# Kernel tuning notes

Measured on AMD Instinct MI355X. Metric: run time of the kernel, lower is better.

Reference implementation:

```python
import jax, jax.numpy as jnp
import numpy as np

B, S, HID = 2, 2048, 2048
NH = 16
HD = HID // NH  # 128


def setup_inputs() -> dict:
    key = jax.random.key(0)
    ks = jax.random.split(key, 9)
    w = 0.02  # init scale to keep logits in a sane range
    return {
        "hidden_states": jax.random.normal(ks[0], (B, S, HID), dtype=jnp.float32),
        "Wq": jax.random.normal(ks[1], (HID, HID), dtype=jnp.float32) * w,
        "bq": jnp.zeros((HID,), dtype=jnp.float32),
        "Wk": jax.random.normal(ks[2], (HID, HD), dtype=jnp.float32) * w,
        "bk": jnp.zeros((HD,), dtype=jnp.float32),
        "Wv": jax.random.normal(ks[3], (HID, HD), dtype=jnp.float32) * w,
        "bv": jnp.zeros((HD,), dtype=jnp.float32),
        "Wo": jax.random.normal(ks[4], (HID, HID), dtype=jnp.float32) * w,
        "bo": jnp.zeros((HID,), dtype=jnp.float32),
    }


def reference(hidden_states, Wq, bq, Wk, bk, Wv, bv, Wo, bo):
    b, s, _ = hidden_states.shape
    # Projections (weights stored [in, out])
    q = hidden_states @ Wq + bq                      # [B,S,HID]
    k = hidden_states @ Wk + bk                      # [B,S,HD] single shared KV head
    v = hidden_states @ Wv + bv                      # [B,S,HD]
    q = q.reshape(b, s, NH, HD)                      # [B,S,H,D]
    # MQA: all query heads attend to the same K/V
    scores = jnp.einsum("bshd,btd->bhst", q, k) / jnp.sqrt(jnp.float32(HD))  # [B,H,S,S]
    probs = jax.nn.softmax(scores, axis=-1)
    attn = jnp.einsum("bhst,btd->bshd", probs, v)    # [B,S,H,D]
    attn = attn.reshape(b, s, HID)
    return attn @ Wo + bo
```

## Files before the change

kernel.cpp:

```cpp
#include <hip/hip_runtime.h>
#include <math.h>

#define BB  2
#define SS  2048
#define HID 2048
#define NH  16
#define HD  128
#define MT  (BB * SS)
#define NC  (HID + 2 * HD)
#define QK_SCALE 0.08838834764831845f

typedef unsigned short ushort_t;
typedef unsigned int uint_t;
typedef __bf16 bf16x8 __attribute__((ext_vector_type(8)));
typedef short short8 __attribute__((ext_vector_type(8)));
typedef float f32x4 __attribute__((ext_vector_type(4)));

__device__ __forceinline__ ushort_t f2bf(float x) {
    union { float f; uint_t u; } a; a.f = x;
    return (ushort_t)((a.u + 0x7FFFu + ((a.u >> 16) & 1u)) >> 16);
}
__device__ __forceinline__ ushort_t f2bf_fast(float x) {
    union { float f; uint_t u; } a; a.f = x;
    return (ushort_t)((a.u + 0x8000u) >> 16);
}

__device__ __forceinline__ int sw_addr(int r, int c) {
    return ((r >> 1) << 6) + ((((((r & 1) << 2) | c)) ^ ((r >> 1) & 7)) << 3);
}

__global__ __launch_bounds__(256) void conv_bf16_kernel(
    const float* __restrict__ in, ushort_t* __restrict__ outb)
{
    const size_t i = ((size_t)blockIdx.x * 256 + threadIdx.x) * 8;
    const float4 a = *(const float4*)&in[i];
    const float4 b = *(const float4*)&in[i + 4];
    short8 o;
    o[0] = (short)f2bf(a.x); o[1] = (short)f2bf(a.y);
    o[2] = (short)f2bf(a.z); o[3] = (short)f2bf(a.w);
    o[4] = (short)f2bf(b.x); o[5] = (short)f2bf(b.y);
    o[6] = (short)f2bf(b.z); o[7] = (short)f2bf(b.w);
    *(short8*)&outb[i] = o;
}

__global__ __launch_bounds__(256) void convT_kernel(
    const float* __restrict__ W, ushort_t* __restrict__ Th, int K, int N)
{
    __shared__ float Ts[64][65];
    const int t = threadIdx.x;
    const int k0 = blockIdx.x * 64, n0 = blockIdx.y * 64;
    const int rr = t >> 4, c4 = (t & 15) * 4;
#pragma unroll
    for (int i = 0; i < 4; i++) {
        const int k = rr + i * 16;
        const float4 v = *(const float4*)&W[(size_t)(k0 + k) * N + n0 + c4];
        Ts[k][c4 + 0] = v.x; Ts[k][c4 + 1] = v.y;
        Ts[k][c4 + 2] = v.z; Ts[k][c4 + 3] = v.w;
    }
    __syncthreads();
    const int n = t >> 2, kc = (t & 3) * 16;
    short8 hv[2];
#pragma unroll
    for (int jj = 0; jj < 16; jj++)
        hv[jj >> 3][jj & 7] = (short)f2bf(Ts[kc + jj][n]);
    const size_t ob = (size_t)(n0 + n) * K + k0 + kc;
    *(short8*)&Th[ob]     = hv[0];
    *(short8*)&Th[ob + 8] = hv[1];
}

__global__ __launch_bounds__(256, 2) void gemm_qkv_kernel(
    const ushort_t* __restrict__ Ab, const ushort_t* __restrict__ WT,
    const float* __restrict__ bq, const float* __restrict__ bk,
    const float* __restrict__ bv,
    ushort_t* __restrict__ qb, ushort_t* __restrict__ kb,
    ushort_t* __restrict__ vtb)
{
    __shared__ short lds[8192];
    constexpr int AH = 0, BH = 4096;
    constexpr int K = HID;
    const int t  = threadIdx.x;
    const int wv = t >> 6, ln = t & 63;
    const int row0 = blockIdx.y * 128, col0 = blockIdx.x * 128;

    size_t agbase[2], bgbase[2];
    int    lbase[2];
#pragma unroll
    for (int i = 0; i < 2; i++) {
        const int I = wv * 2 + i;
        const int lrow = I * 8 + (ln >> 3);
        const int sb = (ln & 7) ^ (lrow & 7);
        const int rr = lrow * 2 + (sb >> 2);
        const int cc = sb & 3;
        agbase[i] = (size_t)(row0 + rr) * K + cc * 8;
        bgbase[i] = (size_t)(col0 + rr) * K + cc * 8;
        lbase[i] = I * 512;
    }

    const int wm0 = (wv & 1) * 64, wn0 = (wv >> 1) * 64;
    const int q = ln >> 4, lm = ln & 15;
    int aoff[4], boff[4];
#pragma unroll
    for (int i = 0; i < 4; i++) aoff[i] = sw_addr(wm0 + i * 16 + lm, q);
#pragma unroll
    for (int j = 0; j < 4; j++) boff[j] = sw_addr(wn0 + j * 16 + lm, q);

    f32x4 acc[4][4];
#pragma unroll
    for (int i = 0; i < 4; i++)
#pragma unroll
        for (int j = 0; j < 4; j++) acc[i][j] = 0.f;

    for (int k0 = 0; k0 < K; k0 += 32) {
        __syncthreads();
#pragma unroll
        for (int i = 0; i < 2; i++) {
            __builtin_amdgcn_global_load_lds(
                (const __attribute__((address_space(1))) void*)(Ab + agbase[i] + k0),
                (__attribute__((address_space(3))) void*)&lds[AH + lbase[i]], 16, 0, 0);
            __builtin_amdgcn_global_load_lds(
                (const __attribute__((address_space(1))) void*)(WT + bgbase[i] + k0),
                (__attribute__((address_space(3))) void*)&lds[BH + lbase[i]], 16, 0, 0);
        }
        __syncthreads();

        bf16x8 ah[4], bh[4];
#pragma unroll
        for (int i = 0; i < 4; i++) ah[i] = *(const bf16x8*)&lds[AH + aoff[i]];
#pragma unroll
        for (int j = 0; j < 4; j++) bh[j] = *(const bf16x8*)&lds[BH + boff[j]];
#pragma unroll
        for (int i = 0; i < 4; i++)
#pragma unroll
            for (int j = 0; j < 4; j++)
                acc[i][j] = __builtin_amdgcn_mfma_f32_16x16x32_bf16(ah[i], bh[j], acc[i][j], 0, 0, 0);
    }

    const int mode = (col0 < HID) ? 0 : ((col0 == HID) ? 1 : 2);
    const float* bsel = (mode == 0) ? bq : ((mode == 1) ? bk : bv);
    const int noff = (mode == 0) ? 0 : ((mode == 1) ? HID : HID + HD);
    float bj[4];
#pragma unroll
    for (int j = 0; j < 4; j++) bj[j] = bsel[col0 - noff + wn0 + j * 16 + lm];
#pragma unroll
    for (int i = 0; i < 4; i++) {
        const int mb = row0 + wm0 + i * 16 + q * 4;
#pragma unroll
        for (int j = 0; j < 4; j++) {
            const int nn = col0 + wn0 + j * 16 + lm;
#pragma unroll
            for (int rr2 = 0; rr2 < 4; rr2++) {
                const float v = acc[i][j][rr2] + bj[j];
                if (mode == 0)      qb [(size_t)(mb + rr2) * HID + nn]           = f2bf_fast(v * QK_SCALE);
                else if (mode == 1) kb [(size_t)(mb + rr2) * HD + (nn - HID)]    = f2bf_fast(v);
                else                vtb[(size_t)(nn - HID - HD) * MT + mb + rr2] = f2bf_fast(v);
            }
        }
    }
}

__global__ __launch_bounds__(256, 2) void gemm_oproj_kernel(
    const ushort_t* __restrict__ Ab, const ushort_t* __restrict__ WT,
    const float* __restrict__ bias, float* __restrict__ C, int M, int N, int K)
{
    __shared__ short lds[8192];
    constexpr int AH = 0, BH = 4096;
    const int t  = threadIdx.x;
    const int wv = t >> 6, ln = t & 63;
    const int row0 = blockIdx.y * 128, col0 = blockIdx.x * 128;

    size_t agbase[2], bgbase[2];
    int    lbase[2];
#pragma unroll
    for (int i = 0; i < 2; i++) {
        const int I = wv * 2 + i;
        const int lrow = I * 8 + (ln >> 3);
        const int sb = (ln & 7) ^ (lrow & 7);
        const int rr = lrow * 2 + (sb >> 2);
        const int cc = sb & 3;
        agbase[i] = (size_t)(row0 + rr) * K + cc * 8;
        bgbase[i] = (size_t)(col0 + rr) * K + cc * 8;
        lbase[i] = I * 512;
    }

    const int wm0 = (wv & 1) * 64, wn0 = (wv >> 1) * 64;
    const int q = ln >> 4, lm = ln & 15;
    int aoff[4], boff[4];
#pragma unroll
    for (int i = 0; i < 4; i++) aoff[i] = sw_addr(wm0 + i * 16 + lm, q);
#pragma unroll
    for (int j = 0; j < 4; j++) boff[j] = sw_addr(wn0 + j * 16 + lm, q);

    f32x4 acc[4][4];
#pragma unroll
    for (int i = 0; i < 4; i++)
#pragma unroll
        for (int j = 0; j < 4; j++) acc[i][j] = 0.f;

    for (int k0 = 0; k0 < K; k0 += 32) {
        __syncthreads();
#pragma unroll
        for (int i = 0; i < 2; i++) {
            __builtin_amdgcn_global_load_lds(
                (const __attribute__((address_space(1))) void*)(Ab + agbase[i] + k0),
                (__attribute__((address_space(3))) void*)&lds[AH + lbase[i]], 16, 0, 0);
            __builtin_amdgcn_global_load_lds(
                (const __attribute__((address_space(1))) void*)(WT + bgbase[i] + k0),
                (__attribute__((address_space(3))) void*)&lds[BH + lbase[i]], 16, 0, 0);
        }
        __syncthreads();

        bf16x8 ah[4], bh[4];
#pragma unroll
        for (int i = 0; i < 4; i++) ah[i] = *(const bf16x8*)&lds[AH + aoff[i]];
#pragma unroll
        for (int j = 0; j < 4; j++) bh[j] = *(const bf16x8*)&lds[BH + boff[j]];
#pragma unroll
        for (int i = 0; i < 4; i++)
#pragma unroll
            for (int j = 0; j < 4; j++)
                acc[i][j] = __builtin_amdgcn_mfma_f32_16x16x32_bf16(ah[i], bh[j], acc[i][j], 0, 0, 0);
    }

    float bj[4];
#pragma unroll
    for (int j = 0; j < 4; j++) bj[j] = bias[col0 + wn0 + j * 16 + lm];
#pragma unroll
    for (int i = 0; i < 4; i++) {
        const int mb = row0 + wm0 + i * 16 + q * 4;
#pragma unroll
        for (int j = 0; j < 4; j++) {
            const int nn = col0 + wn0 + j * 16 + lm;
#pragma unroll
            for (int rr2 = 0; rr2 < 4; rr2++)
                C[(size_t)(mb + rr2) * N + nn] = acc[i][j][rr2] + bj[j];
        }
    }
}

__global__ __launch_bounds__(256, 4) void attn_mfma_kernel(
    const ushort_t* __restrict__ qg, const ushort_t* __restrict__ kg,
    const ushort_t* __restrict__ vtg, ushort_t* Oh)
{
    __shared__ short Ks[8192], Vts[8192], Ps[4096];
    const int b = blockIdx.z, h = blockIdx.y, qt = blockIdx.x;
    const int t = threadIdx.x, wv = t >> 6, ln = t & 63;
    const int q = ln >> 4, lm = ln & 15;
    const int w16 = wv * 16;
    const int am = w16 + lm, amx = am & 15, amx7 = am & 7;

#pragma unroll
    for (int i = 0; i < 4; i++) {
        const int I = wv * 4 + i;
        const int r = 4 * I + (ln >> 4);
        const int c = (ln & 15) ^ (r & 15);
        const ushort_t* src = qg + (size_t)(b * SS + qt * 64 + r) * HID + h * HD + c * 8;
        __builtin_amdgcn_global_load_lds((const __attribute__((address_space(1))) void*)src,
            (__attribute__((address_space(3))) void*)&Ks[I * 512], 16, 0, 0);
    }
    __syncthreads();
    bf16x8 aq[4];
#pragma unroll
    for (int ks = 0; ks < 4; ks++)
        aq[ks] = *(const bf16x8*)&Ks[am * 128 + (((ks << 2) | q) ^ amx) * 8];

    size_t kbase[4], vbase[4];
#pragma unroll
    for (int i = 0; i < 4; i++) {
        const int I = wv * 4 + i;
        { const int r = 4 * I + (ln >> 4); const int c = (ln & 15) ^ (r & 15);
          kbase[i] = (size_t)(b * SS + r) * HD + c * 8; }
        { const int r = 8 * I + (ln >> 3); const int c = (ln & 7) ^ (r & 7);
          vbase[i] = (size_t)r * MT + b * SS + c * 8; }
    }

    float lrow[4] = {0.f, 0.f, 0.f, 0.f};
    f32x4 O[8];
#pragma unroll
    for (int ct = 0; ct < 8; ct++) O[ct] = 0.f;

    for (int kt = 0; kt < SS; kt += 64) {
        __syncthreads();
#pragma unroll
        for (int i = 0; i < 4; i++) {
            const int I = wv * 4 + i;
            __builtin_amdgcn_global_load_lds(
                (const __attribute__((address_space(1))) void*)(kg + kbase[i] + (size_t)kt * HD),
                (__attribute__((address_space(3))) void*)&Ks[I * 512], 16, 0, 0);
            __builtin_amdgcn_global_load_lds(
                (const __attribute__((address_space(1))) void*)(vtg + vbase[i] + kt),
                (__attribute__((address_space(3))) void*)&Vts[I * 512], 16, 0, 0);
        }
        __syncthreads();

        f32x4 s[4];
#pragma unroll
        for (int ct = 0; ct < 4; ct++) s[ct] = 0.f;
#pragma unroll
        for (int ks = 0; ks < 4; ks++) {
#pragma unroll
            for (int ct = 0; ct < 4; ct++) {
                const int n = ct * 16 + lm;
                const bf16x8 bk = *(const bf16x8*)&Ks[n * 128 + (((ks << 2) | q) ^ (n & 15)) * 8];
                s[ct] = __builtin_amdgcn_mfma_f32_16x16x32_bf16(aq[ks], bk, s[ct], 0, 0, 0);
            }
        }

#pragma unroll
        for (int ct = 0; ct < 4; ct++) {
            const int ch = ct * 2 + (lm >> 3);
#pragma unroll
            for (int r = 0; r < 4; r++) {
                const float p = __expf(s[ct][r]);
                lrow[r] += p;
                const int pr = w16 + q * 4 + r;
                Ps[pr * 64 + ((ch ^ (pr & 7)) << 3) + (lm & 7)] = (short)f2bf_fast(p);
            }
        }

#pragma unroll
        for (int ks = 0; ks < 2; ks++) {
            const bf16x8 ap = *(const bf16x8*)&Ps[am * 64 + (((ks << 2) | q) ^ amx7) * 8];
#pragma unroll
            for (int ct = 0; ct < 8; ct++) {
                const int d = ct * 16 + lm;
                const bf16x8 bv = *(const bf16x8*)&Vts[d * 64 + (((ks << 2) | q) ^ (d & 7)) * 8];
                O[ct] = __builtin_amdgcn_mfma_f32_16x16x32_bf16(ap, bv, O[ct], 0, 0, 0);
            }
        }
    }

#pragma unroll
    for (int msk = 1; msk < 16; msk <<= 1)
#pragma unroll
        for (int r = 0; r < 4; r++) lrow[r] += __shfl_xor(lrow[r], msk);
#pragma unroll
    for (int r = 0; r < 4; r++) {
        const float inv = 1.f / lrow[r];
        const size_t base = (size_t)(b * SS + qt * 64 + w16 + q * 4 + r) * HID + h * HD;
#pragma unroll
        for (int ct = 0; ct < 8; ct++)
            Oh[base + ct * 16 + lm] = f2bf_fast(O[ct][r] * inv);
    }
}

extern "C" void kernel_launch(void* const* d_in, const int* in_sizes, int n_in,
                              void* d_out, int out_size, void* d_ws, size_t ws_size,
                              hipStream_t stream)
{
    const float* hs = (const float*)d_in[0];
    const float* Wq = (const float*)d_in[1];
    const float* bq = (const float*)d_in[2];
    const float* Wk = (const float*)d_in[3];
    const float* bk = (const float*)d_in[4];
    const float* Wv = (const float*)d_in[5];
    const float* bv = (const float*)d_in[6];
    const float* Wo = (const float*)d_in[7];
    const float* bo = (const float*)d_in[8];
    float* out = (float*)d_out;

    char* w = (char*)d_ws;
    ushort_t* hsb  = (ushort_t*)w;  w += (size_t)MT * HID * 2;
    ushort_t* qb   = (ushort_t*)w;  w += (size_t)MT * HID * 2;
    ushort_t* kb   = (ushort_t*)w;  w += (size_t)MT * HD * 2;
    ushort_t* vtb  = (ushort_t*)w;  w += (size_t)HD * MT * 2;
    ushort_t* WcT  = (ushort_t*)w;  w += (size_t)NC * HID * 2;
    ushort_t* WoT  = WcT;

    conv_bf16_kernel<<<(MT * HID) / (256 * 8), 256, 0, stream>>>(hs, hsb);
    convT_kernel<<<dim3(HID / 64, HID / 64), 256, 0, stream>>>(Wq, WcT, HID, HID);
    convT_kernel<<<dim3(HID / 64, HD / 64),  256, 0, stream>>>(
        Wk, WcT + (size_t)HID * HID, HID, HD);
    convT_kernel<<<dim3(HID / 64, HD / 64),  256, 0, stream>>>(
        Wv, WcT + (size_t)(HID + HD) * HID, HID, HD);

    gemm_qkv_kernel<<<dim3(NC / 128, MT / 128), 256, 0, stream>>>(
        hsb, WcT, bq, bk, bv, qb, kb, vtb);

    convT_kernel<<<dim3(HID / 64, HID / 64), 256, 0, stream>>>(Wo, WoT, HID, HID);

    attn_mfma_kernel<<<dim3(SS / 64, NH, BB), 256, 0, stream>>>(qb, kb, vtb, qb);

    gemm_oproj_kernel<<<dim3(HID / 128, MT / 128), 256, 0, stream>>>(
        qb, WoT, bo, out, MT, HID, HID);
}
```

Baseline: 323.5 us.

## Double-buffer K/V tiles in attention with async LDS prefetch and MFMA priority

Double-buffers the K and V^T tiles in shared memory so the next tile's global-to-LDS loads are issued before computing on the current tile. A partial vmcnt wait and raw s_barrier replace the two __syncthreads per iteration. s_setprio is raised around the MFMA sections. LDS per block roughly doubles and launch bounds drop from 4 to 2 blocks per CU, trading occupancy for overlap of memory latency.

```diff
diff --git a/kernel.cpp b/kernel.cpp
--- a/kernel.cpp
+++ b/kernel.cpp
@@ -28,6 +28,8 @@
 __device__ __forceinline__ int sw_addr(int r, int c) {
     return ((r >> 1) << 6) + ((((((r & 1) << 2) | c)) ^ ((r >> 1) & 7)) << 3);
 }
+
+#define CFENCE() asm volatile("" ::: "memory")
 
 __global__ __launch_bounds__(256) void conv_bf16_kernel(
     const float* __restrict__ in, ushort_t* __restrict__ outb)
@@ -237,11 +239,11 @@
     }
 }
 
-__global__ __launch_bounds__(256, 4) void attn_mfma_kernel(
+__global__ __launch_bounds__(256, 2) void attn_mfma_kernel(
     const ushort_t* __restrict__ qg, const ushort_t* __restrict__ kg,
     const ushort_t* __restrict__ vtg, ushort_t* Oh)
 {
-    __shared__ short Ks[8192], Vts[8192], Ps[4096];
+    __shared__ short Ks[2][8192], Vts[2][8192], Ps[4096];
     const int b = blockIdx.z, h = blockIdx.y, qt = blockIdx.x;
     const int t = threadIdx.x, wv = t >> 6, ln = t & 63;
     const int q = ln >> 4, lm = ln & 15;
@@ -255,13 +257,14 @@
         const int c = (ln & 15) ^ (r & 15);
         const ushort_t* src = qg + (size_t)(b * SS + qt * 64 + r) * HID + h * HD + c * 8;
         __builtin_amdgcn_global_load_lds((const __attribute__((address_space(1))) void*)src,
-            (__attribute__((address_space(3))) void*)&Ks[I * 512], 16, 0, 0);
+            (__attribute__((address_space(3))) void*)&Ks[0][I * 512], 16, 0, 0);
     }
     __syncthreads();
     bf16x8 aq[4];
 #pragma unroll
     for (int ks = 0; ks < 4; ks++)
-        aq[ks] = *(const bf16x8*)&Ks[am * 128 + (((ks << 2) | q) ^ amx) * 8];
+        aq[ks] = *(const bf16x8*)&Ks[0][am * 128 + (((ks << 2) | q) ^ amx) * 8];
+    __syncthreads();
 
     size_t kbase[4], vbase[4];
 #pragma unroll
@@ -273,37 +276,59 @@
           vbase[i] = (size_t)r * MT + b * SS + c * 8; }
     }
 
+#pragma unroll
+    for (int i = 0; i < 4; i++) {
+        const int I = wv * 4 + i;
+        __builtin_amdgcn_global_load_lds(
+            (const __attribute__((address_space(1))) void*)(kg + kbase[i]),
+            (__attribute__((address_space(3))) void*)&Ks[0][I * 512], 16, 0, 0);
+        __builtin_amdgcn_global_load_lds(
+            (const __attribute__((address_space(1))) void*)(vtg + vbase[i]),
+            (__attribute__((address_space(3))) void*)&Vts[0][I * 512], 16, 0, 0);
+    }
+
     float lrow[4] = {0.f, 0.f, 0.f, 0.f};
     f32x4 O[8];
 #pragma unroll
     for (int ct = 0; ct < 8; ct++) O[ct] = 0.f;
 
     for (int kt = 0; kt < SS; kt += 64) {
-        __syncthreads();
-#pragma unroll
-        for (int i = 0; i < 4; i++) {
-            const int I = wv * 4 + i;
-            __builtin_amdgcn_global_load_lds(
-                (const __attribute__((address_space(1))) void*)(kg + kbase[i] + (size_t)kt * HD),
-                (__attribute__((address_space(3))) void*)&Ks[I * 512], 16, 0, 0);
-            __builtin_amdgcn_global_load_lds(
-                (const __attribute__((address_space(1))) void*)(vtg + vbase[i] + kt),
-                (__attribute__((address_space(3))) void*)&Vts[I * 512], 16, 0, 0);
-        }
-        __syncthreads();
+        const int cur = (kt >> 6) & 1;
+        const int nxt = cur ^ 1;
+
+        if (kt + 64 < SS) {
+#pragma unroll
+            for (int i = 0; i < 4; i++) {
+                const int I = wv * 4 + i;
+                __builtin_amdgcn_global_load_lds(
+                    (const __attribute__((address_space(1))) void*)(kg + kbase[i] + (size_t)(kt + 64) * HD),
+                    (__attribute__((address_space(3))) void*)&Ks[nxt][I * 512], 16, 0, 0);
+                __builtin_amdgcn_global_load_lds(
+                    (const __attribute__((address_space(1))) void*)(vtg + vbase[i] + kt + 64),
+                    (__attribute__((address_space(3))) void*)&Vts[nxt][I * 512], 16, 0, 0);
+            }
+            asm volatile("s_waitcnt vmcnt(8)" ::: "memory");
+        } else {
+            asm volatile("s_waitcnt vmcnt(0)" ::: "memory");
+        }
+        CFENCE();
+        __builtin_amdgcn_s_barrier();
+        CFENCE();
 
         f32x4 s[4];
 #pragma unroll
         for (int ct = 0; ct < 4; ct++) s[ct] = 0.f;
+        __builtin_amdgcn_s_setprio(1);
 #pragma unroll
         for (int ks = 0; ks < 4; ks++) {
 #pragma unroll
             for (int ct = 0; ct < 4; ct++) {
                 const int n = ct * 16 + lm;
-                const bf16x8 bk = *(const bf16x8*)&Ks[n * 128 + (((ks << 2) | q) ^ (n & 15)) * 8];
+                const bf16x8 bk = *(const bf16x8*)&Ks[cur][n * 128 + (((ks << 2) | q) ^ (n & 15)) * 8];
                 s[ct] = __builtin_amdgcn_mfma_f32_16x16x32_bf16(aq[ks], bk, s[ct], 0, 0, 0);
             }
         }
+        __builtin_amdgcn_s_setprio(0);
 
 #pragma unroll
         for (int ct = 0; ct < 4; ct++) {
@@ -317,16 +342,22 @@
             }
         }
 
+        __builtin_amdgcn_s_setprio(1);
 #pragma unroll
         for (int ks = 0; ks < 2; ks++) {
             const bf16x8 ap = *(const bf16x8*)&Ps[am * 64 + (((ks << 2) | q) ^ amx7) * 8];
 #pragma unroll
             for (int ct = 0; ct < 8; ct++) {
                 const int d = ct * 16 + lm;
-                const bf16x8 bv = *(const bf16x8*)&Vts[d * 64 + (((ks << 2) | q) ^ (d & 7)) * 8];
+                const bf16x8 bv = *(const bf16x8*)&Vts[cur][d * 64 + (((ks << 2) | q) ^ (d & 7)) * 8];
                 O[ct] = __builtin_amdgcn_mfma_f32_16x16x32_bf16(ap, bv, O[ct], 0, 0, 0);
             }
         }
+        __builtin_amdgcn_s_setprio(0);
+
+        CFENCE();
+        __builtin_amdgcn_s_barrier();
+        CFENCE();
     }
 
 #pragma unroll
```

New measurement: 337.1 us. 1.04x slower.
